# Optimization experiments

Hardware: AMD Instinct MI355X
Metric: run time of the kernel (lower is better)

The kernel has to match this reference:

```python
import jax, jax.numpy as jnp
import numpy as np

B, DIN, DOUT = 4096, 4096, 4096

def setup_inputs() -> dict:
    key = jax.random.key(0)
    k1, k2, k3 = jax.random.split(key, 3)
    x = jax.random.normal(k1, (B, DIN), dtype=jnp.float32)
    W = jax.random.normal(k2, (DOUT, DIN), dtype=jnp.float32) * 0.01
    alpha = jnp.ones((DOUT, DIN), dtype=jnp.float32) * 0.01
    eta = jnp.asarray(0.1, dtype=jnp.float32)
    bias = jnp.zeros((DOUT,), dtype=jnp.float32)
    return {"x": x, "W": W, "alpha": alpha, "eta": eta, "bias": bias}

def reference(x, W, alpha, eta, bias):
    # y_slow = x @ W.T + b                          (B, DOUT)
    y_slow = jnp.einsum('bi,oi->bo', x, W) + bias
    # x_norm = x / (||x|| + 1e-8)
    x_norm = x / (jnp.linalg.norm(x, axis=-1, keepdims=True) + 1e-8)
    y_pre = jnp.tanh(y_slow)
    # plastic_i = eta * y_pre_i * sum_j sigmoid(alpha)_ij * x_norm_j * x_j
    # (algebraic rewrite of bmm over per-sample outer-product trace; same math)
    s = jnp.einsum('bi,oi->bo', x_norm * x, jax.nn.sigmoid(alpha))  # (B, DOUT)
    plastic = eta * y_pre * s
    return y_slow + plastic
```

## Files before the change

### kernel.cpp

```cpp
#include <hip/hip_runtime.h>
#include <hip/hip_bf16.h>
#include <math.h>


typedef __attribute__((ext_vector_type(4))) float floatx4;
typedef __attribute__((ext_vector_type(8))) short shortx8;
typedef __attribute__((ext_vector_type(4))) int intx4;

#define MAT_N 4096
#define MAT_ELEMS ((size_t)MAT_N * MAT_N)

__device__ __forceinline__ unsigned short f2bf(float f) {
    unsigned int u = __float_as_uint(f);
    unsigned int r = (u + 0x7fffu + ((u >> 16) & 1u)) >> 16;
    return (unsigned short)r;
}

__device__ __forceinline__ void gload_lds16(const void* gptr, void* lptr) {
    __builtin_amdgcn_global_load_lds(
        (const __attribute__((address_space(1))) unsigned int*)gptr,
        (__attribute__((address_space(3))) unsigned int*)lptr,
        16, 0, 0);
}

__device__ __forceinline__ unsigned lds_off(const void* p) {
    return (unsigned)(unsigned long long)(const __attribute__((address_space(3))) char*)p;
}

template <int OFF>
__device__ __forceinline__ intx4 ldsb128(unsigned addr) {
    intx4 d;
    asm volatile("ds_read_b128 %0, %1 offset:%2" : "=v"(d) : "v"(addr), "i"(OFF));
    return d;
}
template <int OFF>
__device__ __forceinline__ long ldsb64(unsigned addr) {
    long d;
    asm volatile("ds_read_b64 %0, %1 offset:%2" : "=v"(d) : "v"(addr), "i"(OFF));
    return d;
}

#define LGKM0() do { asm volatile("s_waitcnt lgkmcnt(0)" ::: "memory"); \
                     __builtin_amdgcn_sched_barrier(0); } while (0)
#define VMCNT(n) asm volatile("s_waitcnt vmcnt(" #n ")" ::: "memory")
#define BARRIER() do { asm volatile("" ::: "memory"); \
                       __builtin_amdgcn_s_barrier(); \
                       asm volatile("" ::: "memory"); } while (0)

__global__ __launch_bounds__(512) void convx_kernel(const float* __restrict__ x,
                                                    unsigned short* __restrict__ xb,
                                                    unsigned char* __restrict__ p8,
                                                    float* __restrict__ sumsq) {
    size_t base = ((size_t)blockIdx.x * 512 + threadIdx.x) * 8;
    const float4* xp = (const float4*)(x + base);
    float4 a = xp[0], b = xp[1];
    float v[8] = {a.x, a.y, a.z, a.w, b.x, b.y, b.z, b.w};
    shortx8 xo;
    float sq[8];
    float s = 0.f;
#pragma unroll
    for (int j = 0; j < 8; j++) {
        xo[j] = (short)f2bf(v[j]);
        sq[j] = v[j] * v[j];
        s += sq[j];
    }
    *(shortx8*)(xb + base) = xo;
    int p0 = __builtin_amdgcn_cvt_pk_fp8_f32(sq[0], sq[1], 0, false);
    p0 = __builtin_amdgcn_cvt_pk_fp8_f32(sq[2], sq[3], p0, true);
    int p1 = __builtin_amdgcn_cvt_pk_fp8_f32(sq[4], sq[5], 0, false);
    p1 = __builtin_amdgcn_cvt_pk_fp8_f32(sq[6], sq[7], p1, true);
    int2 pv = {p0, p1};
    *(int2*)(p8 + base) = pv;
    for (int off = 32; off > 0; off >>= 1) s += __shfl_down(s, off, 64);
    if ((threadIdx.x & 63) == 0) atomicAdd(&sumsq[base >> 12], s);
}

__global__ __launch_bounds__(512) void convwa_kernel(const float* __restrict__ W,
                                                     const float* __restrict__ alpha,
                                                     unsigned short* __restrict__ wb,
                                                     unsigned char* __restrict__ a8) {
    size_t base = ((size_t)blockIdx.x * 512 + threadIdx.x) * 8;
    const float4* wp = (const float4*)(W + base);
    const float4* ap = (const float4*)(alpha + base);
    float4 w0 = wp[0], w1 = wp[1], a0 = ap[0], a1 = ap[1];
    float wv[8] = {w0.x, w0.y, w0.z, w0.w, w1.x, w1.y, w1.z, w1.w};
    float av[8] = {a0.x, a0.y, a0.z, a0.w, a1.x, a1.y, a1.z, a1.w};
    shortx8 wo;
    float sg[8];
#pragma unroll
    for (int j = 0; j < 8; j++) {
        wo[j] = (short)f2bf(wv[j]);
        sg[j] = 1.0f / (1.0f + __expf(-av[j]));
    }
    *(shortx8*)(wb + base) = wo;
    int p0 = __builtin_amdgcn_cvt_pk_fp8_f32(sg[0], sg[1], 0, false);
    p0 = __builtin_amdgcn_cvt_pk_fp8_f32(sg[2], sg[3], p0, true);
    int p1 = __builtin_amdgcn_cvt_pk_fp8_f32(sg[4], sg[5], 0, false);
    p1 = __builtin_amdgcn_cvt_pk_fp8_f32(sg[6], sg[7], p1, true);
    int2 pv = {p0, p1};
    *(int2*)(a8 + base) = pv;
}

__global__ __launch_bounds__(512, 2) void fused_gemm_kernel(
    const unsigned short* __restrict__ X,
    const unsigned short* __restrict__ Wb,
    const unsigned char* __restrict__ P8,
    const unsigned char* __restrict__ A8,
    const float* __restrict__ bias,
    const float* __restrict__ eta_p,
    const float* __restrict__ sumsq,
    float* __restrict__ out) {
    constexpr int K = MAT_N;
    constexpr int N = MAT_N;
    __shared__ __align__(16) unsigned short sX[2][256 * 64];
    __shared__ __align__(16) unsigned short sW[2][128 * 64];
    __shared__ __align__(16) unsigned char  sP[2][256 * 64];
    __shared__ __align__(16) unsigned char  sA[2][128 * 64];

    const int tid = threadIdx.x;
    const int row0 = blockIdx.y * 256;
    const int col0 = blockIdx.x * 128;
    const int lane = tid & 63;
    const int wave = tid >> 6;
    const int wm = (wave >> 1) * 64;
    const int wn = (wave & 1) * 64;
    const int quad = lane >> 4;
    const int l16 = lane & 15;

    floatx4 accY[4][4], accS[4][4];
#pragma unroll
    for (int i = 0; i < 4; i++)
#pragma unroll
        for (int j = 0; j < 4; j++) {
            accY[i][j] = (floatx4){0.f, 0.f, 0.f, 0.f};
            accS[i][j] = (floatx4){0.f, 0.f, 0.f, 0.f};
        }

    const int rs  = tid >> 3;
    const int kcg = (tid & 7) ^ (rs & 7);
    const size_t xrow = (size_t)(row0 + rs) * K + (size_t)kcg * 8;
    const size_t wrow = (size_t)(col0 + rs) * K + (size_t)kcg * 8;
    const int r8 = tid >> 2;
    const int s8 = (2 * (tid & 3)) ^ (r8 & 6);
    const size_t prow = (size_t)(row0 + r8) * K + (size_t)s8 * 8;
    const size_t arow = (size_t)(col0 + r8) * K + (size_t)s8 * 8;

    const unsigned sx0 = lds_off(&sX[0][0]);
    const unsigned sw0 = lds_off(&sW[0][0]);
    const unsigned sp0 = lds_off(&sP[0][0]);
    const unsigned sa0 = lds_off(&sA[0][0]);

#define PF_X(SEG, BUF, KP) gload_lds16(X + xrow + (size_t)(SEG) * 64 * K + (KP), &sX[BUF][(SEG) * 4096 + tid * 8])
#define PF_W(SEG, BUF, KP) gload_lds16(Wb + wrow + (size_t)(SEG) * 64 * K + (KP), &sW[BUF][(SEG) * 4096 + tid * 8])
#define PF_P(SEG, BUF, KP) gload_lds16(P8 + prow + (size_t)(SEG) * 128 * K + (KP), &sP[BUF][(SEG) * 8192 + tid * 16])
#define PF_A8(BUF, KP)     gload_lds16(A8 + arow + (KP), &sA[BUF][tid * 16])

    PF_X(0, 0, 0); PF_X(1, 0, 0); PF_X(2, 0, 0); PF_X(3, 0, 0);
    PF_W(0, 0, 0); PF_W(1, 0, 0);
    PF_P(0, 0, 0); PF_P(1, 0, 0); PF_A8(0, 0);
    VMCNT(3);
    BARRIER();

    for (int t = 0; t < 64; ++t) {
        const int cur = t & 1;
        const int nx = cur ^ 1;
        const size_t kp = (size_t)((t + 1) & 63) * 64;
        const unsigned sxc = sx0 + (unsigned)cur * (256 * 64 * 2);
        const unsigned swc = sw0 + (unsigned)cur * (128 * 64 * 2);
        const unsigned spc = sp0 + (unsigned)cur * (256 * 64);
        const unsigned sac = sa0 + (unsigned)cur * (128 * 64);

        {
            const unsigned kcp = (unsigned)(((0 * 4 + quad) ^ (l16 & 7)) * 16);
            const unsigned ax = sxc + (unsigned)(wm + l16) * 128 + kcp;
            const unsigned bx = swc + (unsigned)(wn + l16) * 128 + kcp;
            intx4 a[4], b[4];
            a[0] = ldsb128<0>(ax); a[1] = ldsb128<2048>(ax);
            a[2] = ldsb128<4096>(ax); a[3] = ldsb128<6144>(ax);
            b[0] = ldsb128<0>(bx); b[1] = ldsb128<2048>(bx);
            b[2] = ldsb128<4096>(bx); b[3] = ldsb128<6144>(bx);
            PF_X(0, nx, kp); PF_X(1, nx, kp); PF_X(2, nx, kp);
            LGKM0();
            __builtin_amdgcn_s_setprio(1);
#pragma unroll
            for (int i = 0; i < 4; ++i)
#pragma unroll
                for (int j = 0; j < 4; ++j)
                    accY[i][j] = __builtin_amdgcn_mfma_f32_16x16x32_bf16(
                        __builtin_bit_cast(shortx8, a[i]),
                        __builtin_bit_cast(shortx8, b[j]), accY[i][j], 0, 0, 0);
            __builtin_amdgcn_s_setprio(0);
            BARRIER();
        }
        {
            const unsigned kcp = (unsigned)(((1 * 4 + quad) ^ (l16 & 7)) * 16);
            const unsigned ax = sxc + (unsigned)(wm + l16) * 128 + kcp;
            const unsigned bx = swc + (unsigned)(wn + l16) * 128 + kcp;
            intx4 a[4], b[4];
            a[0] = ldsb128<0>(ax); a[1] = ldsb128<2048>(ax);
            a[2] = ldsb128<4096>(ax); a[3] = ldsb128<6144>(ax);
            b[0] = ldsb128<0>(bx); b[1] = ldsb128<2048>(bx);
            b[2] = ldsb128<4096>(bx); b[3] = ldsb128<6144>(bx);
            PF_X(3, nx, kp); PF_W(0, nx, kp); PF_W(1, nx, kp);
            LGKM0();
            __builtin_amdgcn_s_setprio(1);
#pragma unroll
            for (int i = 0; i < 4; ++i)
#pragma unroll
                for (int j = 0; j < 4; ++j)
                    accY[i][j] = __builtin_amdgcn_mfma_f32_16x16x32_bf16(
                        __builtin_bit_cast(shortx8, a[i]),
                        __builtin_bit_cast(shortx8, b[j]), accY[i][j], 0, 0, 0);
            __builtin_amdgcn_s_setprio(0);
            VMCNT(6);
            BARRIER();
        }
        {
            const unsigned lsp = (unsigned)(((0 * 4 + quad) ^ (l16 & 6)) * 8);
            const unsigned px = spc + (unsigned)(wm + l16) * 64 + lsp;
            const unsigned qx = sac + (unsigned)(wn + l16) * 64 + lsp;
            long p[4], q[4];
            p[0] = ldsb64<0>(px); p[1] = ldsb64<1024>(px);
            p[2] = ldsb64<2048>(px); p[3] = ldsb64<3072>(px);
            q[0] = ldsb64<0>(qx); q[1] = ldsb64<1024>(qx);
            q[2] = ldsb64<2048>(qx); q[3] = ldsb64<3072>(qx);
            PF_P(0, nx, kp); PF_P(1, nx, kp);
            LGKM0();
            __builtin_amdgcn_s_setprio(1);
#pragma unroll
            for (int i = 0; i < 4; ++i)
#pragma unroll
                for (int j = 0; j < 4; ++j)
                    accS[i][j] = __builtin_amdgcn_mfma_f32_16x16x32_fp8_fp8(
                        p[i], q[j], accS[i][j], 0, 0, 0);
            __builtin_amdgcn_s_setprio(0);
            BARRIER();
        }
        {
            const unsigned lsp = (unsigned)(((1 * 4 + quad) ^ (l16 & 6)) * 8);
            const unsigned px = spc + (unsigned)(wm + l16) * 64 + lsp;
            const unsigned qx = sac + (unsigned)(wn + l16) * 64 + lsp;
            long p[4], q[4];
            p[0] = ldsb64<0>(px); p[1] = ldsb64<1024>(px);
            p[2] = ldsb64<2048>(px); p[3] = ldsb64<3072>(px);
            q[0] = ldsb64<0>(qx); q[1] = ldsb64<1024>(qx);
            q[2] = ldsb64<2048>(qx); q[3] = ldsb64<3072>(qx);
            PF_A8(nx, kp);
            LGKM0();
            __builtin_amdgcn_s_setprio(1);
#pragma unroll
            for (int i = 0; i < 4; ++i)
#pragma unroll
                for (int j = 0; j < 4; ++j)
                    accS[i][j] = __builtin_amdgcn_mfma_f32_16x16x32_fp8_fp8(
                        p[i], q[j], accS[i][j], 0, 0, 0);
            __builtin_amdgcn_s_setprio(0);
            VMCNT(3);
            BARRIER();
        }
    }
    VMCNT(0);

    const float eta = *eta_p;
#pragma unroll
    for (int i = 0; i < 4; i++) {
#pragma unroll
        for (int r = 0; r < 4; r++) {
            const int grow = row0 + wm + i * 16 + quad * 4 + r;
            const float invn = 1.0f / (sqrtf(sumsq[grow]) + 1e-8f);
#pragma unroll
            for (int j = 0; j < 4; j++) {
                const int gcol = col0 + wn + j * 16 + l16;
                float y = accY[i][j][r] + bias[gcol];
                float s = accS[i][j][r] * invn;
                out[(size_t)grow * N + gcol] = y + eta * tanhf(y) * s;
            }
        }
    }
}

extern "C" void kernel_launch(void* const* d_in, const int* in_sizes, int n_in,
                              void* d_out, int out_size, void* d_ws, size_t ws_size,
                              hipStream_t stream) {
    const float* x     = (const float*)d_in[0];
    const float* W     = (const float*)d_in[1];
    const float* alpha = (const float*)d_in[2];
    const float* eta   = (const float*)d_in[3];
    const float* bias  = (const float*)d_in[4];
    float* out = (float*)d_out;

    char* ws = (char*)d_ws;
    float* sumsq = (float*)ws;
    unsigned short* xb = (unsigned short*)(ws + 16384);
    unsigned short* wb = xb + MAT_ELEMS;
    unsigned char*  p8 = (unsigned char*)(wb + MAT_ELEMS);
    unsigned char*  a8 = p8 + MAT_ELEMS;

    hipMemsetAsync(sumsq, 0, MAT_N * sizeof(float), stream);
    convx_kernel<<<MAT_ELEMS / (8 * 512), 512, 0, stream>>>(x, xb, p8, sumsq);
    convwa_kernel<<<MAT_ELEMS / (8 * 512), 512, 0, stream>>>(W, alpha, wb, a8);

    dim3 grid(MAT_N / 128, MAT_N / 256);
    fused_gemm_kernel<<<grid, 512, 0, stream>>>(xb, wb, p8, a8, bias, eta, sumsq, out);
}
```

Baseline: 430.3 us.

## Derive fp8 squared-x operand in registers from bf16 X fragments

```diff
diff --git a/kernel.cpp b/kernel.cpp
--- a/kernel.cpp
+++ b/kernel.cpp
@@ -14,6 +14,10 @@
     unsigned int u = __float_as_uint(f);
     unsigned int r = (u + 0x7fffu + ((u >> 16) & 1u)) >> 16;
     return (unsigned short)r;
+}
+
+__device__ __forceinline__ float bf2f(unsigned short h) {
+    return __uint_as_float((unsigned int)h << 16);
 }
 
 __device__ __forceinline__ void gload_lds16(const void* gptr, void* lptr) {
@@ -47,30 +51,38 @@
                        __builtin_amdgcn_s_barrier(); \
                        asm volatile("" ::: "memory"); } while (0)
 
+__device__ __forceinline__ long sq8_fp8(shortx8 v) {
+    float s0 = bf2f((unsigned short)v[0]); s0 *= s0;
+    float s1 = bf2f((unsigned short)v[1]); s1 *= s1;
+    float s2 = bf2f((unsigned short)v[2]); s2 *= s2;
+    float s3 = bf2f((unsigned short)v[3]); s3 *= s3;
+    float s4 = bf2f((unsigned short)v[4]); s4 *= s4;
+    float s5 = bf2f((unsigned short)v[5]); s5 *= s5;
+    float s6 = bf2f((unsigned short)v[6]); s6 *= s6;
+    float s7 = bf2f((unsigned short)v[7]); s7 *= s7;
+    int p0 = __builtin_amdgcn_cvt_pk_fp8_f32(s0, s1, 0, false);
+    p0 = __builtin_amdgcn_cvt_pk_fp8_f32(s2, s3, p0, true);
+    int p1 = __builtin_amdgcn_cvt_pk_fp8_f32(s4, s5, 0, false);
+    p1 = __builtin_amdgcn_cvt_pk_fp8_f32(s6, s7, p1, true);
+    int2 r = {p0, p1};
+    return __builtin_bit_cast(long, r);
+}
+
 __global__ __launch_bounds__(512) void convx_kernel(const float* __restrict__ x,
                                                     unsigned short* __restrict__ xb,
-                                                    unsigned char* __restrict__ p8,
                                                     float* __restrict__ sumsq) {
     size_t base = ((size_t)blockIdx.x * 512 + threadIdx.x) * 8;
     const float4* xp = (const float4*)(x + base);
     float4 a = xp[0], b = xp[1];
     float v[8] = {a.x, a.y, a.z, a.w, b.x, b.y, b.z, b.w};
     shortx8 xo;
-    float sq[8];
     float s = 0.f;
 #pragma unroll
     for (int j = 0; j < 8; j++) {
         xo[j] = (short)f2bf(v[j]);
-        sq[j] = v[j] * v[j];
-        s += sq[j];
+        s += v[j] * v[j];
     }
     *(shortx8*)(xb + base) = xo;
-    int p0 = __builtin_amdgcn_cvt_pk_fp8_f32(sq[0], sq[1], 0, false);
-    p0 = __builtin_amdgcn_cvt_pk_fp8_f32(sq[2], sq[3], p0, true);
-    int p1 = __builtin_amdgcn_cvt_pk_fp8_f32(sq[4], sq[5], 0, false);
-    p1 = __builtin_amdgcn_cvt_pk_fp8_f32(sq[6], sq[7], p1, true);
-    int2 pv = {p0, p1};
-    *(int2*)(p8 + base) = pv;
     for (int off = 32; off > 0; off >>= 1) s += __shfl_down(s, off, 64);
     if ((threadIdx.x & 63) == 0) atomicAdd(&sumsq[base >> 12], s);
 }
@@ -104,7 +116,6 @@
 __global__ __launch_bounds__(512, 2) void fused_gemm_kernel(
     const unsigned short* __restrict__ X,
     const unsigned short* __restrict__ Wb,
-    const unsigned char* __restrict__ P8,
     const unsigned char* __restrict__ A8,
     const float* __restrict__ bias,
     const float* __restrict__ eta_p,
@@ -114,7 +125,6 @@
     constexpr int N = MAT_N;
     __shared__ __align__(16) unsigned short sX[2][256 * 64];
     __shared__ __align__(16) unsigned short sW[2][128 * 64];
-    __shared__ __align__(16) unsigned char  sP[2][256 * 64];
     __shared__ __align__(16) unsigned char  sA[2][128 * 64];
 
     const int tid = threadIdx.x;
@@ -142,24 +152,23 @@
     const size_t wrow = (size_t)(col0 + rs) * K + (size_t)kcg * 8;
     const int r8 = tid >> 2;
     const int s8 = (2 * (tid & 3)) ^ (r8 & 6);
-    const size_t prow = (size_t)(row0 + r8) * K + (size_t)s8 * 8;
     const size_t arow = (size_t)(col0 + r8) * K + (size_t)s8 * 8;
 
     const unsigned sx0 = lds_off(&sX[0][0]);
     const unsigned sw0 = lds_off(&sW[0][0]);
-    const unsigned sp0 = lds_off(&sP[0][0]);
     const unsigned sa0 = lds_off(&sA[0][0]);
 
 #define PF_X(SEG, BUF, KP) gload_lds16(X + xrow + (size_t)(SEG) * 64 * K + (KP), &sX[BUF][(SEG) * 4096 + tid * 8])
 #define PF_W(SEG, BUF, KP) gload_lds16(Wb + wrow + (size_t)(SEG) * 64 * K + (KP), &sW[BUF][(SEG) * 4096 + tid * 8])
-#define PF_P(SEG, BUF, KP) gload_lds16(P8 + prow + (size_t)(SEG) * 128 * K + (KP), &sP[BUF][(SEG) * 8192 + tid * 16])
 #define PF_A8(BUF, KP)     gload_lds16(A8 + arow + (KP), &sA[BUF][tid * 16])
 
     PF_X(0, 0, 0); PF_X(1, 0, 0); PF_X(2, 0, 0); PF_X(3, 0, 0);
     PF_W(0, 0, 0); PF_W(1, 0, 0);
-    PF_P(0, 0, 0); PF_P(1, 0, 0); PF_A8(0, 0);
-    VMCNT(3);
+    PF_A8(0, 0);
+    VMCNT(0);
     BARRIER();
+
+    long p0f[4], p1f[4];
 
     for (int t = 0; t < 64; ++t) {
         const int cur = t & 1;
@@ -167,7 +176,6 @@
         const size_t kp = (size_t)((t + 1) & 63) * 64;
         const unsigned sxc = sx0 + (unsigned)cur * (256 * 64 * 2);
         const unsigned swc = sw0 + (unsigned)cur * (128 * 64 * 2);
-        const unsigned spc = sp0 + (unsigned)cur * (256 * 64);
         const unsigned sac = sa0 + (unsigned)cur * (128 * 64);
 
         {
@@ -190,7 +198,9 @@
                         __builtin_bit_cast(shortx8, a[i]),
                         __builtin_bit_cast(shortx8, b[j]), accY[i][j], 0, 0, 0);
             __builtin_amdgcn_s_setprio(0);
-            BARRIER();
+#pragma unroll
+            for (int i = 0; i < 4; ++i)
+                p0f[i] = sq8_fp8(__builtin_bit_cast(shortx8, a[i]));
         }
         {
             const unsigned kcp = (unsigned)(((1 * 4 + quad) ^ (l16 & 7)) * 16);
@@ -212,39 +222,27 @@
                         __builtin_bit_cast(shortx8, a[i]),
                         __builtin_bit_cast(shortx8, b[j]), accY[i][j], 0, 0, 0);
             __builtin_amdgcn_s_setprio(0);
+#pragma unroll
+            for (int i = 0; i < 4; ++i)
+                p1f[i] = sq8_fp8(__builtin_bit_cast(shortx8, a[i]));
             VMCNT(6);
             BARRIER();
         }
         {
-            const unsigned lsp = (unsigned)(((0 * 4 + quad) ^ (l16 & 6)) * 8);
-            const unsigned px = spc + (unsigned)(wm + l16) * 64 + lsp;
-            const unsigned qx = sac + (unsigned)(wn + l16) * 64 + lsp;
-            long p[4], q[4];
-            p[0] = ldsb64<0>(px); p[1] = ldsb64<1024>(px);
-            p[2] = ldsb64<2048>(px); p[3] = ldsb64<3072>(px);
-            q[0] = ldsb64<0>(qx); q[1] = ldsb64<1024>(qx);
-            q[2] = ldsb64<2048>(qx); q[3] = ldsb64<3072>(qx);
-            PF_P(0, nx, kp); PF_P(1, nx, kp);
-            LGKM0();
-            __builtin_amdgcn_s_setprio(1);
-#pragma unroll
-            for (int i = 0; i < 4; ++i)
-#pragma unroll
-                for (int j = 0; j < 4; ++j)
-                    accS[i][j] = __builtin_amdgcn_mfma_f32_16x16x32_fp8_fp8(
-                        p[i], q[j], accS[i][j], 0, 0, 0);
-            __builtin_amdgcn_s_setprio(0);
-            BARRIER();
-        }
-        {
-            const unsigned lsp = (unsigned)(((1 * 4 + quad) ^ (l16 & 6)) * 8);
-            const unsigned px = spc + (unsigned)(wm + l16) * 64 + lsp;
-            const unsigned qx = sac + (unsigned)(wn + l16) * 64 + lsp;
-            long p[4], q[4];
-            p[0] = ldsb64<0>(px); p[1] = ldsb64<1024>(px);
-            p[2] = ldsb64<2048>(px); p[3] = ldsb64<3072>(px);
-            q[0] = ldsb64<0>(qx); q[1] = ldsb64<1024>(qx);
-            q[2] = ldsb64<2048>(qx); q[3] = ldsb64<3072>(qx);
+            const unsigned lsp0 = (unsigned)(((0 * 4 + quad) ^ (l16 & 6)) * 8);
+            const unsigned lsp1 = (unsigned)(((1 * 4 + quad) ^ (l16 & 6)) * 8);
+            const unsigned qxb = sac + (unsigned)(wn + l16) * 64;
+            long q0[4], q1[4];
+            {
+                const unsigned qx0 = qxb + lsp0;
+                q0[0] = ldsb64<0>(qx0); q0[1] = ldsb64<1024>(qx0);
+                q0[2] = ldsb64<2048>(qx0); q0[3] = ldsb64<3072>(qx0);
+            }
+            {
+                const unsigned qx1 = qxb + lsp1;
+                q1[0] = ldsb64<0>(qx1); q1[1] = ldsb64<1024>(qx1);
+                q1[2] = ldsb64<2048>(qx1); q1[3] = ldsb64<3072>(qx1);
+            }
             PF_A8(nx, kp);
             LGKM0();
             __builtin_amdgcn_s_setprio(1);
@@ -253,9 +251,15 @@
 #pragma unroll
                 for (int j = 0; j < 4; ++j)
                     accS[i][j] = __builtin_amdgcn_mfma_f32_16x16x32_fp8_fp8(
-                        p[i], q[j], accS[i][j], 0, 0, 0);
+                        p0f[i], q0[j], accS[i][j], 0, 0, 0);
+#pragma unroll
+            for (int i = 0; i < 4; ++i)
+#pragma unroll
+                for (int j = 0; j < 4; ++j)
+                    accS[i][j] = __builtin_amdgcn_mfma_f32_16x16x32_fp8_fp8(
+                        p1f[i], q1[j], accS[i][j], 0, 0, 0);
             __builtin_amdgcn_s_setprio(0);
-            VMCNT(3);
+            VMCNT(1);
             BARRIER();
         }
     }
@@ -293,13 +297,12 @@
     float* sumsq = (float*)ws;
     unsigned short* xb = (unsigned short*)(ws + 16384);
     unsigned short* wb = xb + MAT_ELEMS;
-    unsigned char*  p8 = (unsigned char*)(wb + MAT_ELEMS);
-    unsigned char*  a8 = p8 + MAT_ELEMS;
+    unsigned char*  a8 = (unsigned char*)(wb + MAT_ELEMS);
 
     hipMemsetAsync(sumsq, 0, MAT_N * sizeof(float), stream);
-    convx_kernel<<<MAT_ELEMS / (8 * 512), 512, 0, stream>>>(x, xb, p8, sumsq);
+    convx_kernel<<<MAT_ELEMS / (8 * 512), 512, 0, stream>>>(x, xb, sumsq);
     convwa_kernel<<<MAT_ELEMS / (8 * 512), 512, 0, stream>>>(W, alpha, wb, a8);
 
     dim3 grid(MAT_N / 128, MAT_N / 256);
-    fused_gemm_kernel<<<grid, 512, 0, stream>>>(xb, wb, p8, a8, bias, eta, sumsq, out);
-}
+    fused_gemm_kernel<<<grid, 512, 0, stream>>>(xb, wb, a8, bias, eta, sumsq, out);
+}
```

Result: slower. 466.0 us (+8.3%).
